# Optimization experiments

Measured on AMD Instinct MI355X. Metric: run time of the kernel, lower is better.

The kernel has to match this reference:

```python
import jax, jax.numpy as jnp
import numpy as np

HIDDEN = 2048
Q_HEADS = 16
KV_HEADS = 4
HEAD_DIM = HIDDEN // Q_HEADS  # 128
GROUPS = Q_HEADS // KV_HEADS  # 4


def setup_inputs() -> dict:
    key = jax.random.key(0)
    ks = jax.random.split(key, 5)
    scale = 1.0 / np.sqrt(HIDDEN)
    x = jax.random.normal(ks[0], (1, 4096, HIDDEN), dtype=jnp.float32)
    # nn.Linear weights stored as [out_features, in_features]
    Wq = jax.random.uniform(ks[1], (Q_HEADS * HEAD_DIM, HIDDEN), jnp.float32, -scale, scale)
    Wk = jax.random.uniform(ks[2], (KV_HEADS * HEAD_DIM, HIDDEN), jnp.float32, -scale, scale)
    Wv = jax.random.uniform(ks[3], (KV_HEADS * HEAD_DIM, HIDDEN), jnp.float32, -scale, scale)
    Wo = jax.random.uniform(ks[4], (HIDDEN, HIDDEN), jnp.float32, -scale, scale)
    return {"x": x, "Wq": Wq, "Wk": Wk, "Wv": Wv, "Wo": Wo}


def reference(x, Wq, Wk, Wv, Wo):
    b, s, _ = x.shape
    norm = jnp.asarray(np.sqrt(HEAD_DIM), x.dtype)
    # Projections (Linear without bias: x @ W.T)
    q = (x @ Wq.T).reshape(b, s, KV_HEADS, GROUPS, HEAD_DIM)  # group q heads by shared kv head
    k = (x @ Wk.T).reshape(b, s, KV_HEADS, HEAD_DIM)
    v = (x @ Wv.T).reshape(b, s, KV_HEADS, HEAD_DIM)
    # Scores: repeat_interleave of KV is equivalent to sharing k across the g axis
    att = jnp.einsum('bskgd,btkd->bkgst', q, k) / norm  # [b,kv,groups,s,s]
    att = jax.nn.softmax(att, axis=-1)
    out = jnp.einsum('bkgst,btkd->bskgd', att, v).reshape(b, s, HIDDEN)
    return out @ Wo.T
```

## Files before the change

kernel.cpp:

```cpp
#include <hip/hip_runtime.h>
#include <stdint.h>

#define SEQ 4096
#define HID 2048

typedef __attribute__((ext_vector_type(8))) short short8;
typedef __attribute__((ext_vector_type(4))) float f32x4;
typedef __attribute__((ext_vector_type(16))) float f32x16;
typedef unsigned int u32;
typedef __attribute__((ext_vector_type(4))) u32 u32x4;

__device__ __forceinline__ short bf16_rne(float f) {
  u32 u = __builtin_bit_cast(u32, f);
  u += 0x7FFFu + ((u >> 16) & 1u);
  return (short)(u >> 16);
}

__device__ __forceinline__ void gload16(const void* gp, void* lp) {
  __builtin_amdgcn_global_load_lds(
      (const __attribute__((address_space(1))) u32*)(uintptr_t)gp,
      (__attribute__((address_space(3))) u32*)(uintptr_t)lp, 16, 0, 0);
}

__global__ __launch_bounds__(256) void cast_bf16(const float* __restrict__ in,
                                                 short* __restrict__ out, int n8,
                                                 float scale) {
  int i = blockIdx.x * 256 + threadIdx.x;
  if (i >= n8) return;
  const f32x4* p = (const f32x4*)in + (size_t)i * 2;
  f32x4 a = p[0], b = p[1];
  short8 o;
#pragma unroll
  for (int j = 0; j < 4; ++j) { o[j] = bf16_rne(a[j] * scale); o[j + 4] = bf16_rne(b[j] * scale); }
  *((short8*)out + i) = o;
}

__global__ __launch_bounds__(256) void cast_w(const float* __restrict__ Wq,
                                              const float* __restrict__ Wk,
                                              const float* __restrict__ Wv,
                                              const float* __restrict__ Wo,
                                              short* __restrict__ wqkv,
                                              short* __restrict__ wob, float qscale) {
  int i = blockIdx.x * 256 + threadIdx.x;
  const float* src;
  short* dst;
  float s = 1.0f;
  int off;
  if (i < 524288) {
    src = Wq; dst = wqkv; off = i; s = qscale;
  } else if (i < 655360) {
    src = Wk; dst = wqkv + (size_t)2048 * 2048; off = i - 524288;
  } else if (i < 786432) {
    src = Wv; dst = wqkv + (size_t)2560 * 2048; off = i - 655360;
  } else {
    src = Wo; dst = wob; off = i - 786432;
  }
  const f32x4* p = (const f32x4*)src + (size_t)off * 2;
  f32x4 a = p[0], b = p[1];
  short8 o;
#pragma unroll
  for (int j = 0; j < 4; ++j) { o[j] = bf16_rne(a[j] * s); o[j + 4] = bf16_rne(b[j] * s); }
  *((short8*)dst + off) = o;
}

__global__ __launch_bounds__(256) void transpose_v(const short* __restrict__ qkv,
                                                   short* __restrict__ vt) {
  __shared__ __align__(16) short tile[64][72];
  int rb = blockIdx.x * 64, cb = blockIdx.y * 64;
  int tid = threadIdx.x;
  int tr = tid >> 3, tc = (tid & 7) * 8;
#pragma unroll
  for (int i = 0; i < 2; ++i)
    *(short8*)&tile[tr + i * 32][tc] =
        *(const short8*)&qkv[(size_t)(rb + tr + i * 32) * 3072 + 2560 + cb + tc];
  __syncthreads();
#pragma unroll
  for (int i = 0; i < 2; ++i) {
    int c = tr + i * 32;
    short8 v;
#pragma unroll
    for (int j = 0; j < 8; ++j) {
      int pos = tc + j;
      int tl = (pos & ~15) | (pos & 3) | ((pos & 4) << 1) | ((pos & 8) >> 1);
      v[j] = tile[tl][c];
    }
    *(short8*)&vt[(size_t)(cb + c) * SEQ + rb + tc] = v;
  }
}

template <typename CT>
__global__ __launch_bounds__(256, 2) void gemm_nt(const short* __restrict__ A,
                                                  const short* __restrict__ B,
                                                  CT* __restrict__ C, int M, int N, int K) {
  __shared__ __align__(16) short As[128 * 32];
  __shared__ __align__(16) short Bs[128 * 32];
  int tid = threadIdx.x, wave = tid >> 6, lane = tid & 63;
  int lr = lane & 15, lg = lane >> 4;
  int wr = wave >> 1, wc = wave & 1;
  size_t rowA0 = (size_t)blockIdx.y * 128, colB0 = (size_t)blockIdx.x * 128;
  f32x4 acc[4][4] = {};

  for (int kt = 0; kt < K; kt += 32) {
#pragma unroll
    for (int c = 0; c < 2; ++c) {
      int chunk = wave * 2 + c;
      int row = chunk * 16 + (lane >> 2);
      int col = (lane & 3) * 8;
      gload16(A + (rowA0 + row) * (size_t)K + kt + col, &As[chunk * 512]);
      gload16(B + (colB0 + row) * (size_t)K + kt + col, &Bs[chunk * 512]);
    }
    __syncthreads();
    short8 a[4], b[4];
#pragma unroll
    for (int i = 0; i < 4; ++i) {
      a[i] = *(const short8*)&As[(wr * 64 + i * 16 + lr) * 32 + lg * 8];
      b[i] = *(const short8*)&Bs[(wc * 64 + i * 16 + lr) * 32 + lg * 8];
    }
#pragma unroll
    for (int i = 0; i < 4; ++i)
#pragma unroll
      for (int j = 0; j < 4; ++j)
        acc[i][j] = __builtin_amdgcn_mfma_f32_16x16x32_bf16(a[i], b[j], acc[i][j], 0, 0, 0);
    __syncthreads();
  }
#pragma unroll
  for (int i = 0; i < 4; ++i)
#pragma unroll
    for (int j = 0; j < 4; ++j)
#pragma unroll
      for (int r = 0; r < 4; ++r) {
        size_t row = rowA0 + wr * 64 + i * 16 + lg * 4 + r;
        size_t col = colB0 + wc * 64 + j * 16 + lr;
        if constexpr (sizeof(CT) == 2) C[row * N + col] = (CT)bf16_rne(acc[i][j][r]);
        else C[row * N + col] = acc[i][j][r];
      }
}

__global__ __launch_bounds__(256, 2) void attn_kernel(const short* __restrict__ QKV,
                                                      const short* __restrict__ Vt,
                                                      short* __restrict__ Oat) {
  __shared__ __align__(16) short Ks[2][4096];
  __shared__ __align__(16) short Vs[2][4096];
  int tid = threadIdx.x, wave = tid >> 6, lane = tid & 63;
  int l31 = lane & 31, hi = lane >> 5;
  int h = blockIdx.y, kv = h >> 2;
  int q0 = blockIdx.x * 128 + wave * 32;

  short8 qf[8];
#pragma unroll
  for (int kb = 0; kb < 8; ++kb)
    qf[kb] = *(const short8*)&QKV[(size_t)(q0 + l31) * 3072 + h * 128 + kb * 16 + hi * 8];

  f32x16 oacc[4] = {};
  float lsum = 0.f;

  const short* Kbase = QKV + 2048 + kv * 128;

  auto stageK = [&](int b, int t0) {
#pragma unroll
    for (int cc = 0; cc < 2; ++cc) {
      int c = wave * 2 + cc;
      gload16(Kbase + (size_t)(t0 + l31) * 3072 + c * 16 + hi * 8, &Ks[b][c * 512]);
    }
  };
  auto stageV = [&](int b, int t0) {
#pragma unroll
    for (int cc = 0; cc < 2; ++cc) {
      int c = wave * 2 + cc;
      int d = (c & 1) * 64 + lane;
      gload16(Vt + (size_t)(kv * 128 + d) * SEQ + t0 + (c >> 1) * 8, &Vs[b][c * 512]);
    }
  };

  stageK(0, 0);
  stageV(0, 0);
  __syncthreads();
  int buf = 0;

  for (int t0 = 0; t0 < SEQ; t0 += 32) {
    int tn = (t0 + 32 < SEQ) ? t0 + 32 : 0;
    stageK(buf ^ 1, tn);
    stageV(buf ^ 1, tn);

    f32x16 sa = {}, sb = {};
    __builtin_amdgcn_s_setprio(1);
#pragma unroll
    for (int kb = 0; kb < 4; ++kb) {
      short8 kfa = *(const short8*)&Ks[buf][((kb * 2 + hi) * 32 + l31) * 8];
      short8 kfb = *(const short8*)&Ks[buf][(((kb + 4) * 2 + hi) * 32 + l31) * 8];
      sa = __builtin_amdgcn_mfma_f32_32x32x16_bf16(kfa, qf[kb], sa, 0, 0, 0);
      sb = __builtin_amdgcn_mfma_f32_32x32x16_bf16(kfb, qf[kb + 4], sb, 0, 0, 0);
    }
    __builtin_amdgcn_s_setprio(0);

    float pp[8];
    u32 w[8];
#pragma unroll
    for (int ii = 0; ii < 8; ++ii) {
      float p0 = __builtin_amdgcn_exp2f(sa[2 * ii] + sb[2 * ii]);
      float p1 = __builtin_amdgcn_exp2f(sa[2 * ii + 1] + sb[2 * ii + 1]);
      pp[ii] = p0 + p1;
      asm("v_cvt_pk_bf16_f32 %0, %1, %2" : "=v"(w[ii]) : "v"(p0), "v"(p1));
    }
    lsum += ((pp[0] + pp[1]) + (pp[2] + pp[3])) + ((pp[4] + pp[5]) + (pp[6] + pp[7]));
    short8 pa0 = __builtin_bit_cast(short8, (u32x4){w[0], w[1], w[2], w[3]});
    short8 pa1 = __builtin_bit_cast(short8, (u32x4){w[4], w[5], w[6], w[7]});

    __builtin_amdgcn_s_setprio(1);
#pragma unroll
    for (int nb = 0; nb < 4; ++nb) {
      short8 v0 = *(const short8*)&Vs[buf][((hi)*128 + nb * 32 + l31) * 8];
      oacc[nb] = __builtin_amdgcn_mfma_f32_32x32x16_bf16(pa0, v0, oacc[nb], 0, 0, 0);
    }
#pragma unroll
    for (int nb = 0; nb < 4; ++nb) {
      short8 v1 = *(const short8*)&Vs[buf][((2 + hi) * 128 + nb * 32 + l31) * 8];
      oacc[nb] = __builtin_amdgcn_mfma_f32_32x32x16_bf16(pa1, v1, oacc[nb], 0, 0, 0);
    }
    __builtin_amdgcn_s_setprio(0);

    __syncthreads();
    buf ^= 1;
  }

  lsum += __shfl_xor(lsum, 32);
  float linv = 1.f / lsum;
#pragma unroll
  for (int r = 0; r < 16; ++r) {
    int qrow = (r & 3) + 8 * (r >> 2) + 4 * hi;
    float lr_ = __shfl(linv, qrow);
#pragma unroll
    for (int nb = 0; nb < 4; ++nb)
      Oat[(size_t)(q0 + qrow) * HID + h * 128 + nb * 32 + l31] = bf16_rne(oacc[nb][r] * lr_);
  }
}

extern "C" void kernel_launch(void* const* d_in, const int* in_sizes, int n_in,
                              void* d_out, int out_size, void* d_ws, size_t ws_size,
                              hipStream_t stream) {
  const float* x = (const float*)d_in[0];
  const float* Wq = (const float*)d_in[1];
  const float* Wk = (const float*)d_in[2];
  const float* Wv = (const float*)d_in[3];
  const float* Wo = (const float*)d_in[4];
  float* out = (float*)d_out;
  char* ws = (char*)d_ws;

  short* xb = (short*)(ws);
  short* wqkv = (short*)(ws + (16u << 20));
  short* wob = (short*)(ws + (28u << 20));
  short* qkv = (short*)(ws + (36u << 20));
  short* vt = wqkv;
  short* oat = xb;

  const float QSCALE = 0.12753102964551932f;

  cast_bf16<<<4096, 256, 0, stream>>>(x, xb, 1048576, 1.0f);
  cast_w<<<5120, 256, 0, stream>>>(Wq, Wk, Wv, Wo, wqkv, wob, QSCALE);

  gemm_nt<short><<<dim3(24, 32), 256, 0, stream>>>(xb, wqkv, qkv, 4096, 3072, 2048);
  transpose_v<<<dim3(64, 8), 256, 0, stream>>>(qkv, vt);
  attn_kernel<<<dim3(32, 16), 256, 0, stream>>>(qkv, vt, oat);
  gemm_nt<float><<<dim3(16, 32), 256, 0, stream>>>(oat, wob, out, 4096, HID, 2048);
}
```

Measured before the change: 275.1 us.

## Fuse V transpose into QKV GEMM epilogue and merge cast kernels

Merges the x and weight cast kernels into one launch, and removes the separate V transpose kernel. The QKV GEMM blocks that cover V columns now write their tile straight into the transposed Vt buffer in the permuted position order the attention kernel expects. This drops one launch and one extra read/write pass of V. In exchange those blocks do strided scattered 2-byte stores along the sequence dimension, which may coalesce poorly, and Vt moves to a separate workspace region.

```diff
diff --git a/kernel.cpp b/kernel.cpp
--- a/kernel.cpp
+++ b/kernel.cpp
@@ -22,38 +22,29 @@
       (__attribute__((address_space(3))) u32*)(uintptr_t)lp, 16, 0, 0);
 }
 
-__global__ __launch_bounds__(256) void cast_bf16(const float* __restrict__ in,
-                                                 short* __restrict__ out, int n8,
-                                                 float scale) {
-  int i = blockIdx.x * 256 + threadIdx.x;
-  if (i >= n8) return;
-  const f32x4* p = (const f32x4*)in + (size_t)i * 2;
-  f32x4 a = p[0], b = p[1];
-  short8 o;
-#pragma unroll
-  for (int j = 0; j < 4; ++j) { o[j] = bf16_rne(a[j] * scale); o[j + 4] = bf16_rne(b[j] * scale); }
-  *((short8*)out + i) = o;
-}
-
-__global__ __launch_bounds__(256) void cast_w(const float* __restrict__ Wq,
-                                              const float* __restrict__ Wk,
-                                              const float* __restrict__ Wv,
-                                              const float* __restrict__ Wo,
-                                              short* __restrict__ wqkv,
-                                              short* __restrict__ wob, float qscale) {
+__global__ __launch_bounds__(256) void cast_all(const float* __restrict__ x,
+                                                const float* __restrict__ Wq,
+                                                const float* __restrict__ Wk,
+                                                const float* __restrict__ Wv,
+                                                const float* __restrict__ Wo,
+                                                short* __restrict__ xb,
+                                                short* __restrict__ wqkv,
+                                                short* __restrict__ wob, float qscale) {
   int i = blockIdx.x * 256 + threadIdx.x;
   const float* src;
   short* dst;
   float s = 1.0f;
   int off;
-  if (i < 524288) {
-    src = Wq; dst = wqkv; off = i; s = qscale;
-  } else if (i < 655360) {
-    src = Wk; dst = wqkv + (size_t)2048 * 2048; off = i - 524288;
-  } else if (i < 786432) {
-    src = Wv; dst = wqkv + (size_t)2560 * 2048; off = i - 655360;
+  if (i < 1048576) {
+    src = x; dst = xb; off = i;
+  } else if (i < 1572864) {
+    src = Wq; dst = wqkv; off = i - 1048576; s = qscale;
+  } else if (i < 1703936) {
+    src = Wk; dst = wqkv + (size_t)2048 * 2048; off = i - 1572864;
+  } else if (i < 1835008) {
+    src = Wv; dst = wqkv + (size_t)2560 * 2048; off = i - 1703936;
   } else {
-    src = Wo; dst = wob; off = i - 786432;
+    src = Wo; dst = wob; off = i - 1835008;
   }
   const f32x4* p = (const f32x4*)src + (size_t)off * 2;
   f32x4 a = p[0], b = p[1];
@@ -63,35 +54,11 @@
   *((short8*)dst + off) = o;
 }
 
-__global__ __launch_bounds__(256) void transpose_v(const short* __restrict__ qkv,
-                                                   short* __restrict__ vt) {
-  __shared__ __align__(16) short tile[64][72];
-  int rb = blockIdx.x * 64, cb = blockIdx.y * 64;
-  int tid = threadIdx.x;
-  int tr = tid >> 3, tc = (tid & 7) * 8;
-#pragma unroll
-  for (int i = 0; i < 2; ++i)
-    *(short8*)&tile[tr + i * 32][tc] =
-        *(const short8*)&qkv[(size_t)(rb + tr + i * 32) * 3072 + 2560 + cb + tc];
-  __syncthreads();
-#pragma unroll
-  for (int i = 0; i < 2; ++i) {
-    int c = tr + i * 32;
-    short8 v;
-#pragma unroll
-    for (int j = 0; j < 8; ++j) {
-      int pos = tc + j;
-      int tl = (pos & ~15) | (pos & 3) | ((pos & 4) << 1) | ((pos & 8) >> 1);
-      v[j] = tile[tl][c];
-    }
-    *(short8*)&vt[(size_t)(cb + c) * SEQ + rb + tc] = v;
-  }
-}
-
-template <typename CT>
+template <typename CT, bool FUSE_VT>
 __global__ __launch_bounds__(256, 2) void gemm_nt(const short* __restrict__ A,
                                                   const short* __restrict__ B,
-                                                  CT* __restrict__ C, int M, int N, int K) {
+                                                  CT* __restrict__ C, int M, int N, int K,
+                                                  short* __restrict__ vt) {
   __shared__ __align__(16) short As[128 * 32];
   __shared__ __align__(16) short Bs[128 * 32];
   int tid = threadIdx.x, wave = tid >> 6, lane = tid & 63;
@@ -122,6 +89,23 @@
       for (int j = 0; j < 4; ++j)
         acc[i][j] = __builtin_amdgcn_mfma_f32_16x16x32_bf16(a[i], b[j], acc[i][j], 0, 0, 0);
     __syncthreads();
+  }
+
+  if constexpr (FUSE_VT) {
+    if (colB0 >= 2560) {
+      int lgp = ((lg & 1) << 1) | (lg >> 1);
+#pragma unroll
+      for (int i = 0; i < 4; ++i)
+#pragma unroll
+        for (int j = 0; j < 4; ++j)
+#pragma unroll
+          for (int r = 0; r < 4; ++r) {
+            size_t d = colB0 - 2560 + wc * 64 + j * 16 + lr;
+            size_t pos = rowA0 + wr * 64 + i * 16 + lgp * 4 + r;
+            vt[d * SEQ + pos] = bf16_rne(acc[i][j][r]);
+          }
+      return;
+    }
   }
 #pragma unroll
   for (int i = 0; i < 4; ++i)
@@ -250,16 +234,15 @@
   short* wqkv = (short*)(ws + (16u << 20));
   short* wob = (short*)(ws + (28u << 20));
   short* qkv = (short*)(ws + (36u << 20));
-  short* vt = wqkv;
+  short* vt = (short*)(ws + (60u << 20));
   short* oat = xb;
 
   const float QSCALE = 0.12753102964551932f;
 
-  cast_bf16<<<4096, 256, 0, stream>>>(x, xb, 1048576, 1.0f);
-  cast_w<<<5120, 256, 0, stream>>>(Wq, Wk, Wv, Wo, wqkv, wob, QSCALE);
-
-  gemm_nt<short><<<dim3(24, 32), 256, 0, stream>>>(xb, wqkv, qkv, 4096, 3072, 2048);
-  transpose_v<<<dim3(64, 8), 256, 0, stream>>>(qkv, vt);
+  cast_all<<<9216, 256, 0, stream>>>(x, Wq, Wk, Wv, Wo, xb, wqkv, wob, QSCALE);
+
+  gemm_nt<short, true><<<dim3(24, 32), 256, 0, stream>>>(xb, wqkv, qkv, 4096, 3072, 2048, vt);
   attn_kernel<<<dim3(32, 16), 256, 0, stream>>>(qkv, vt, oat);
-  gemm_nt<float><<<dim3(16, 32), 256, 0, stream>>>(oat, wob, out, 4096, HID, 2048);
-}
+  gemm_nt<float, false><<<dim3(16, 32), 256, 0, stream>>>(oat, wob, out, 4096, HID, 2048,
+                                                          nullptr);
+}
```

Result: faster. 269.0 us (median of 2 runs) (-2.2%).
